# Optimization experiments

Measured on AMD Instinct MI355X. Metric: run time of the kernel, lower is better.

Reference implementation:

```python
import jax, jax.numpy as jnp
import numpy as np

N_NODES = 100000
N_EDGES = 1600000
IN_CH = 128
HID = 128
OUT_CH = 16
N_GRAPHS = 64


def setup_inputs() -> dict:
    key = jax.random.key(0)
    ks = jax.random.split(key, 8)
    x = jax.random.normal(ks[0], (N_NODES, IN_CH), dtype=jnp.float32)
    edge_index = jax.random.randint(ks[1], (2, N_EDGES), 0, N_NODES, dtype=jnp.int64)
    batch = jnp.sort(jax.random.randint(ks[2], (N_NODES,), 0, N_GRAPHS, dtype=jnp.int64))
    s1 = 1.0 / np.sqrt(IN_CH)
    s2 = 1.0 / np.sqrt(HID)
    W1 = jax.random.uniform(ks[3], (IN_CH, HID), jnp.float32, -s1, s1)
    b1 = jnp.zeros((HID,), jnp.float32)
    W2 = jax.random.uniform(ks[4], (HID, HID), jnp.float32, -s2, s2)
    b2 = jnp.zeros((HID,), jnp.float32)
    Wfc = jax.random.uniform(ks[5], (HID, OUT_CH), jnp.float32, -s2, s2)
    bfc = jax.random.uniform(ks[6], (OUT_CH,), jnp.float32, -s2, s2)
    return {"x": x, "W1": W1, "b1": b1, "W2": W2, "b2": b2,
            "Wfc": Wfc, "bfc": bfc, "edge_index": edge_index, "batch": batch}


def _gcn_conv(x, W, b, src, dst, deg_inv_sqrt, deg_inv):
    # GCNConv with self-loops: out = D^-1/2 (A+I) D^-1/2 (x W) + b
    h = x @ W                                   # [N, H]
    norm = deg_inv_sqrt[src] * deg_inv_sqrt[dst]  # [E]
    agg = jax.ops.segment_sum(h[src] * norm[:, None], dst, num_segments=N_NODES)
    # self-loop term: deg_inv_sqrt[i]^2 * h[i]
    return agg + h * deg_inv[:, None] + b


def reference(x, W1, b1, W2, b2, Wfc, bfc, edge_index, batch):
    src, dst = edge_index[0], edge_index[1]
    # degree including self-loop
    deg = jax.ops.segment_sum(jnp.ones((N_EDGES,), jnp.float32), dst, num_segments=N_NODES) + 1.0
    deg_inv_sqrt = jax.lax.rsqrt(deg)
    deg_inv = 1.0 / deg
    h = jax.nn.relu(_gcn_conv(x, W1, b1, src, dst, deg_inv_sqrt, deg_inv))
    h = jax.nn.relu(_gcn_conv(h, W2, b2, src, dst, deg_inv_sqrt, deg_inv))
    # global mean pool over graphs
    sums = jax.ops.segment_sum(h, batch, num_segments=N_GRAPHS)          # [G, H]
    counts = jax.ops.segment_sum(jnp.ones((N_NODES,), jnp.float32), batch, num_segments=N_GRAPHS)
    pooled = sums / jnp.maximum(counts, 1.0)[:, None]
    return pooled @ Wfc + bfc
```

## Files before the change

kernel.cpp:

```cpp
#include <hip/hip_runtime.h>
#include <math.h>

#define NN 100000
#define NE 1600000
#define CH 128
#define OUTC 16
#define NG 64

#define CBSH 8
#define NCB 391
#define CHK 4096
#define CAP 5120
#define NPW 8

typedef __attribute__((ext_vector_type(8))) short bf16x8;
typedef __attribute__((ext_vector_type(4))) float f32x4;

__device__ __forceinline__ unsigned short f2bf(float f) {
    union { float f; unsigned u; } v; v.f = f;
    unsigned r = v.u + 0x7FFF + ((v.u >> 16) & 1);
    return (unsigned short)(r >> 16);
}
__device__ __forceinline__ float bflo(unsigned u) {
    union { unsigned u; float f; } v; v.u = u << 16; return v.f;
}
__device__ __forceinline__ float bfhi(unsigned u) {
    union { unsigned u; float f; } v; v.u = u & 0xffff0000u; return v.f;
}

__device__ __forceinline__ float2 node_agg(const unsigned* __restrict__ base,
        const int* __restrict__ rowst, const int* __restrict__ degi,
        const int* __restrict__ csr, const float* __restrict__ dis,
        float bb0, float bb1, int n, int lane) {
    unsigned sv = base[(size_t)n * 64 + lane];
    float a0[8], a1[8];
    a0[0] = bflo(sv); a1[0] = bfhi(sv);
#pragma unroll
    for (int u = 1; u < 8; u++) { a0[u] = 0.f; a1[u] = 0.f; }
    int start = __builtin_amdgcn_readfirstlane(rowst[n]);
    int c = __builtin_amdgcn_readfirstlane(degi[n]);
    int j = 0;
    for (; j + 7 < c; j += 8) {
        int idx[8];
#pragma unroll
        for (int u = 0; u < 8; u++) idx[u] = csr[start + j + u];
        unsigned v[8];
#pragma unroll
        for (int u = 0; u < 8; u++) v[u] = base[(size_t)idx[u] * 64 + lane];
#pragma unroll
        for (int u = 0; u < 8; u++) { a0[u] += bflo(v[u]); a1[u] += bfhi(v[u]); }
    }
    for (; j < c; j++) {
        unsigned v0 = base[(size_t)csr[start + j] * 64 + lane];
        a0[j & 7] += bflo(v0); a1[j & 7] += bfhi(v0);
    }
#pragma unroll
    for (int off = 4; off >= 1; off >>= 1)
#pragma unroll
        for (int u = 0; u < off; u++) { a0[u] += a0[u + off]; a1[u] += a1[u + off]; }
    float d = dis[n];
    float ox = fmaxf(fmaf(d, a0[0], bb0), 0.f);
    float oy = fmaxf(fmaf(d, a1[0], bb1), 0.f);
    return make_float2(ox, oy);
}

__global__ void k_prep(const float* __restrict__ W1, const float* __restrict__ W2,
                       unsigned short* __restrict__ wt1, unsigned short* __restrict__ wt2,
                       const int* __restrict__ batch, int* __restrict__ gptr,
                       int* __restrict__ gfill, float* __restrict__ pooled) {
    int i = blockIdx.x * 256 + threadIdx.x;
    if (i < CH * CH) {
        int k = i >> 7, n = i & 127;
        wt1[n * CH + k] = f2bf(W1[i]);
    } else if (i < 2 * CH * CH) {
        int j = i - CH * CH;
        int k = j >> 7, n = j & 127;
        wt2[n * CH + k] = f2bf(W2[j]);
    }
    if (i < NCB) gfill[i] = 0;
    if (i < NG * CH) pooled[i] = 0.f;
    if (i < NN) {
        int b = batch[i];
        int prev = (i == 0) ? -1 : batch[i - 1];
        for (int g = prev + 1; g <= b; g++) gptr[g] = i;
        if (i == NN - 1) {
            for (int g = b + 1; g <= NG; g++) gptr[g] = NN;
        }
    }
}

__global__ __launch_bounds__(1024) void k_passA(const int* __restrict__ src, const int* __restrict__ dst,
                        int* __restrict__ gfill, unsigned* __restrict__ ebuf) {
    __shared__ unsigned lbuf[CHK];
    __shared__ unsigned short lb16[CHK];
    __shared__ int hcnt[NCB];
    __shared__ int hbase[512];
    __shared__ int goff[NCB];
    int t = threadIdx.x;
    if (t < NCB) hcnt[t] = 0;
    __syncthreads();
    int base = blockIdx.x * CHK;
    int cb[4], slot[4]; unsigned pk[4];
#pragma unroll
    for (int i = 0; i < 4; i++) {
        int e = base + i * 1024 + t;
        cb[i] = -1;
        if (e < NE) {
            int d = dst[e], s = src[e];
            cb[i] = d >> CBSH;
            pk[i] = ((unsigned)s << CBSH) | (unsigned)(d & (( 1 << CBSH) - 1));
            slot[i] = atomicAdd(&hcnt[cb[i]], 1);
        }
    }
    __syncthreads();
    if (t < 512) hbase[t] = (t < NCB) ? hcnt[t] : 0;
    __syncthreads();
    for (int off = 1; off < 512; off <<= 1) {
        int v = 0;
        if (t < 512 && t >= off) v = hbase[t - off];
        __syncthreads();
        if (t < 512) hbase[t] += v;
        __syncthreads();
    }
    if (t < NCB) {
        int c = hcnt[t];
        int g = c ? atomicAdd(&gfill[t], c) : 0;
        goff[t] = t * CAP + g - (hbase[t] - c);
    }
    __syncthreads();
#pragma unroll
    for (int i = 0; i < 4; i++) {
        if (cb[i] >= 0) {
            int pos = hbase[cb[i]] - hcnt[cb[i]] + slot[i];
            lbuf[pos] = pk[i];
            lb16[pos] = (unsigned short)cb[i];
        }
    }
    __syncthreads();
    int total = min(NE - base, CHK);
    for (int p = t; p < total; p += 1024) {
        unsigned v = lbuf[p];
        int b = lb16[p];
        ebuf[goff[b] + p] = v;
    }
}

__global__ __launch_bounds__(1024) void k_passB(const unsigned* __restrict__ ebuf, const int* __restrict__ gfill,
                        int* __restrict__ degi, int* __restrict__ rowst,
                        float* __restrict__ dis, int* __restrict__ csr) {
    __shared__ int cnt[256];
    __shared__ int nbase[256];
    __shared__ int fill[256];
    __shared__ int stage[CAP];
    int t = threadIdx.x;
    int cb = blockIdx.x;
    int nb0 = cb << CBSH;
    int ncnt = min(256, NN - nb0);
    int e0 = cb * CAP;
    int e1 = e0 + gfill[cb];
    if (t < 256) { cnt[t] = 0; fill[t] = 0; }
    __syncthreads();
    for (int e = e0 + t; e < e1; e += 1024)
        atomicAdd(&cnt[ebuf[e] & ((1 << CBSH) - 1)], 1);
    __syncthreads();
    if (t < 256) nbase[t] = cnt[t];
    __syncthreads();
    for (int off = 1; off < 256; off <<= 1) {
        int v = 0;
        if (t < 256 && t >= off) v = nbase[t - off];
        __syncthreads();
        if (t < 256) nbase[t] += v;
        __syncthreads();
    }
    for (int e = e0 + t; e < e1; e += 1024) {
        unsigned v = ebuf[e];
        int local = v & ((1 << CBSH) - 1);
        int s = atomicAdd(&fill[local], 1);
        stage[nbase[local] - cnt[local] + s] = (int)(v >> CBSH);
    }
    __syncthreads();
    int total = e1 - e0;
    for (int p = t; p < total; p += 1024) csr[e0 + p] = stage[p];
    if (t < ncnt) {
        int c = cnt[t];
        degi[nb0 + t] = c;
        rowst[nb0 + t] = e0 + nbase[t] - c;
        dis[nb0 + t] = rsqrtf((float)c + 1.0f);
    }
}

template<bool F32IN>
__launch_bounds__(256, 2)
__global__ void k_gemm(const void* __restrict__ Av,
                       const unsigned short* __restrict__ WT,
                       const float* __restrict__ dis,
                       unsigned short* __restrict__ out) {
    int tid = threadIdx.x;
    int wave = tid >> 6, lane = tid & 63;
    int quad = lane >> 4, l16 = lane & 15;

    int rbase = blockIdx.x * 128 + wave * 32;

    bf16x8 af[2][4];
#pragma unroll
    for (int s = 0; s < 2; s++) {
        int row = rbase + s * 16 + l16;
        if (row >= NN) row = NN - 1;
        if (F32IN) {
            const float* arow = (const float*)Av + (size_t)row * CH + quad * 8;
#pragma unroll
            for (int ks = 0; ks < 4; ks++) {
                float4 lo = *(const float4*)(arow + ks * 32);
                float4 hi = *(const float4*)(arow + ks * 32 + 4);
                union { bf16x8 v; unsigned short u[8]; } tmp;
                tmp.u[0] = f2bf(lo.x); tmp.u[1] = f2bf(lo.y);
                tmp.u[2] = f2bf(lo.z); tmp.u[3] = f2bf(lo.w);
                tmp.u[4] = f2bf(hi.x); tmp.u[5] = f2bf(hi.y);
                tmp.u[6] = f2bf(hi.z); tmp.u[7] = f2bf(hi.w);
                af[s][ks] = tmp.v;
            }
        } else {
            const unsigned short* arow = (const unsigned short*)Av + (size_t)row * CH + quad * 8;
#pragma unroll
            for (int ks = 0; ks < 4; ks++) af[s][ks] = *(const bf16x8*)(arow + ks * 32);
        }
    }

    f32x4 acc[2][8];
#pragma unroll
    for (int s = 0; s < 2; s++)
#pragma unroll
        for (int t = 0; t < 8; t++) acc[s][t] = (f32x4){0.f, 0.f, 0.f, 0.f};

#pragma unroll
    for (int t = 0; t < 8; t++) {
        const unsigned short* wcol = WT + (size_t)(t * 16 + l16) * CH + quad * 8;
        bf16x8 b0 = *(const bf16x8*)(wcol);
        bf16x8 b1 = *(const bf16x8*)(wcol + 32);
        bf16x8 b2 = *(const bf16x8*)(wcol + 64);
        bf16x8 b3 = *(const bf16x8*)(wcol + 96);
#pragma unroll
        for (int s = 0; s < 2; s++) {
            acc[s][t] = __builtin_amdgcn_mfma_f32_16x16x32_bf16(af[s][0], b0, acc[s][t], 0, 0, 0);
            acc[s][t] = __builtin_amdgcn_mfma_f32_16x16x32_bf16(af[s][1], b1, acc[s][t], 0, 0, 0);
            acc[s][t] = __builtin_amdgcn_mfma_f32_16x16x32_bf16(af[s][2], b2, acc[s][t], 0, 0, 0);
            acc[s][t] = __builtin_amdgcn_mfma_f32_16x16x32_bf16(af[s][3], b3, acc[s][t], 0, 0, 0);
        }
    }

#pragma unroll
    for (int s = 0; s < 2; s++) {
#pragma unroll
        for (int r = 0; r < 4; r++) {
            int orow = rbase + s * 16 + quad * 4 + r;
            if (orow < NN) {
                float d = dis[orow];
#pragma unroll
                for (int t = 0; t < 8; t++) {
                    out[(size_t)orow * CH + t * 16 + l16] = f2bf(acc[s][t][r] * d);
                }
            }
        }
    }
}

__global__ void k_agg(const unsigned short* __restrict__ ht, const int* __restrict__ rowst,
                      const int* __restrict__ degi, const int* __restrict__ csr,
                      const float* __restrict__ dis, const float* __restrict__ bias,
                      unsigned short* __restrict__ out) {
    int wave = threadIdx.x >> 6;
    int lane = threadIdx.x & 63;
    int n = blockIdx.x * 4 + wave;
    if (n >= NN) return;
    const unsigned* base = (const unsigned*)ht;
    float bb0 = bias[lane * 2], bb1 = bias[lane * 2 + 1];
    float2 o = node_agg(base, rowst, degi, csr, dis, bb0, bb1, n, lane);
    unsigned pk = ((unsigned)f2bf(o.y) << 16) | (unsigned)f2bf(o.x);
    ((unsigned*)out)[(size_t)n * 64 + lane] = pk;
}

__global__ void k_aggpool(const unsigned short* __restrict__ ht,
                          const int* __restrict__ rowst, const int* __restrict__ degi,
                          const int* __restrict__ csr, const float* __restrict__ dis,
                          const float* __restrict__ b2, const int* __restrict__ batch,
                          float* __restrict__ pooled) {
    int wave = threadIdx.x >> 6;
    int lane = threadIdx.x & 63;
    int n0 = (blockIdx.x * 4 + wave) * NPW;
    if (n0 >= NN) return;
    int n1 = n0 + NPW; if (n1 > NN) n1 = NN;
    const unsigned* base = (const unsigned*)ht;
    float bb0 = b2[lane * 2], bb1 = b2[lane * 2 + 1];
    float p0 = 0.f, p1 = 0.f;
    int gcur = __builtin_amdgcn_readfirstlane(batch[n0]);
    for (int n = n0; n < n1; n++) {
        int g = __builtin_amdgcn_readfirstlane(batch[n]);
        if (g != gcur) {
            atomicAdd(&pooled[gcur * CH + lane * 2],     p0);
            atomicAdd(&pooled[gcur * CH + lane * 2 + 1], p1);
            p0 = 0.f; p1 = 0.f; gcur = g;
        }
        float2 o = node_agg(base, rowst, degi, csr, dis, bb0, bb1, n, lane);
        p0 += o.x; p1 += o.y;
    }
    atomicAdd(&pooled[gcur * CH + lane * 2],     p0);
    atomicAdd(&pooled[gcur * CH + lane * 2 + 1], p1);
}

__global__ void k_final(const float* __restrict__ pooled, const int* __restrict__ gptr,
                        const float* __restrict__ Wfc, const float* __restrict__ bfc,
                        float* __restrict__ out) {
    int idx = blockIdx.x * 256 + threadIdx.x;
    if (idx >= NG * OUTC) return;
    int g = idx >> 4, o = idx & 15;
    float c = (float)(gptr[g + 1] - gptr[g]);
    float inv = 1.0f / fmaxf(c, 1.0f);
    float s = 0.f;
    for (int k = 0; k < CH; k++) s += pooled[g * CH + k] * Wfc[k * OUTC + o];
    out[idx] = fmaf(s, inv, bfc[o]);
}

extern "C" void kernel_launch(void* const* d_in, const int* in_sizes, int n_in,
                              void* d_out, int out_size, void* d_ws, size_t ws_size,
                              hipStream_t stream) {
    (void)in_sizes; (void)n_in; (void)out_size; (void)ws_size;
    const float* x   = (const float*)d_in[0];
    const float* W1  = (const float*)d_in[1];
    const float* b1  = (const float*)d_in[2];
    const float* W2  = (const float*)d_in[3];
    const float* b2  = (const float*)d_in[4];
    const float* Wfc = (const float*)d_in[5];
    const float* bfc = (const float*)d_in[6];
    const int* ei    = (const int*)d_in[7];
    const int* batch = (const int*)d_in[8];
    const int* esrc = ei;
    const int* edst = ei + NE;
    float* out = (float*)d_out;

    char* w = (char*)d_ws;
    unsigned short* bufA = (unsigned short*)w; w += (size_t)NN * CH * 2;
    unsigned short* bufB = (unsigned short*)w; w += (size_t)NN * CH * 2;
    unsigned short* wt1  = (unsigned short*)w; w += (size_t)CH * CH * 2;
    unsigned short* wt2  = (unsigned short*)w; w += (size_t)CH * CH * 2;
    unsigned* ebuf = (unsigned*)w; w += (size_t)NCB * CAP * 4;
    int* csr    = (int*)w;    w += (size_t)NCB * CAP * 4;
    int* degi   = (int*)w;    w += (size_t)NN * 4;
    int* rowst  = (int*)w;    w += (size_t)NN * 4;
    float* dis  = (float*)w;  w += (size_t)NN * 4;
    int* gfill  = (int*)w;    w += NCB * 4;
    int* gptr   = (int*)w;    w += (NG + 1) * 4;
    float* pooled = (float*)w; w += (size_t)NG * CH * 4;

    const int sortBlocks = (NE + CHK - 1) / CHK;
    const int rowBlocks  = (NN + 127) / 128;
    const int poolBlocks = (NN + 4 * NPW - 1) / (4 * NPW);

    k_prep<<<(NN + 255) / 256, 256, 0, stream>>>(W1, W2, wt1, wt2, batch, gptr, gfill, pooled);
    k_passA<<<sortBlocks, 1024, 0, stream>>>(esrc, edst, gfill, ebuf);
    k_passB<<<NCB, 1024, 0, stream>>>(ebuf, gfill, degi, rowst, dis, csr);

    k_gemm<true><<<rowBlocks, 256, 0, stream>>>(x, wt1, dis, bufA);
    k_agg<<<NN / 4, 256, 0, stream>>>(bufA, rowst, degi, csr, dis, b1, bufB);
    k_gemm<false><<<rowBlocks, 256, 0, stream>>>(bufB, wt2, dis, bufA);
    k_aggpool<<<poolBlocks, 256, 0, stream>>>(bufA, rowst, degi, csr, dis, b2, batch, pooled);

    k_final<<<(NG * OUTC + 255) / 256, 256, 0, stream>>>(pooled, gptr, Wfc, bfc, out);
}
```

Baseline: 334.3 us.

## Pad CSR rows to multiples of eight with a zero dummy node

Each CSR row is padded to a multiple of 8 entries whose index points at an extra zeroed row appended to bufA. The gather loop then always runs in full unrolled groups of 8 and the scalar tail loop is dropped. It also halves NPW, so the pooling aggregation launches more blocks with fewer nodes per wave. The cost is extra padded gathers of the dummy row, a larger CSR buffer and more shared memory in passB.

```diff
diff --git a/kernel.cpp b/kernel.cpp
--- a/kernel.cpp
+++ b/kernel.cpp
@@ -11,7 +11,8 @@
 #define NCB 391
 #define CHK 4096
 #define CAP 5120
-#define NPW 8
+#define CAPP 7168
+#define NPW 4
 
 typedef __attribute__((ext_vector_type(8))) short bf16x8;
 typedef __attribute__((ext_vector_type(4))) float f32x4;
@@ -39,8 +40,8 @@
     for (int u = 1; u < 8; u++) { a0[u] = 0.f; a1[u] = 0.f; }
     int start = __builtin_amdgcn_readfirstlane(rowst[n]);
     int c = __builtin_amdgcn_readfirstlane(degi[n]);
-    int j = 0;
-    for (; j + 7 < c; j += 8) {
+    int cp = (c + 7) & ~7;
+    for (int j = 0; j < cp; j += 8) {
         int idx[8];
 #pragma unroll
         for (int u = 0; u < 8; u++) idx[u] = csr[start + j + u];
@@ -49,10 +50,6 @@
         for (int u = 0; u < 8; u++) v[u] = base[(size_t)idx[u] * 64 + lane];
 #pragma unroll
         for (int u = 0; u < 8; u++) { a0[u] += bflo(v[u]); a1[u] += bfhi(v[u]); }
-    }
-    for (; j < c; j++) {
-        unsigned v0 = base[(size_t)csr[start + j] * 64 + lane];
-        a0[j & 7] += bflo(v0); a1[j & 7] += bfhi(v0);
     }
 #pragma unroll
     for (int off = 4; off >= 1; off >>= 1)
@@ -67,7 +64,8 @@
 __global__ void k_prep(const float* __restrict__ W1, const float* __restrict__ W2,
                        unsigned short* __restrict__ wt1, unsigned short* __restrict__ wt2,
                        const int* __restrict__ batch, int* __restrict__ gptr,
-                       int* __restrict__ gfill, float* __restrict__ pooled) {
+                       int* __restrict__ gfill, float* __restrict__ pooled,
+                       unsigned* __restrict__ bufAz) {
     int i = blockIdx.x * 256 + threadIdx.x;
     if (i < CH * CH) {
         int k = i >> 7, n = i & 127;
@@ -79,6 +77,7 @@
     }
     if (i < NCB) gfill[i] = 0;
     if (i < NG * CH) pooled[i] = 0.f;
+    if (i < 64) bufAz[(size_t)NN * 64 + i] = 0;
     if (i < NN) {
         int b = batch[i];
         int prev = (i == 0) ? -1 : batch[i - 1];
@@ -108,7 +107,7 @@
         if (e < NE) {
             int d = dst[e], s = src[e];
             cb[i] = d >> CBSH;
-            pk[i] = ((unsigned)s << CBSH) | (unsigned)(d & (( 1 << CBSH) - 1));
+            pk[i] = ((unsigned)s << CBSH) | (unsigned)(d & ((1 << CBSH) - 1));
             slot[i] = atomicAdd(&hcnt[cb[i]], 1);
         }
     }
@@ -149,9 +148,9 @@
                         int* __restrict__ degi, int* __restrict__ rowst,
                         float* __restrict__ dis, int* __restrict__ csr) {
     __shared__ int cnt[256];
-    __shared__ int nbase[256];
+    __shared__ int pb[256];
     __shared__ int fill[256];
-    __shared__ int stage[CAP];
+    __shared__ int stage[CAPP];
     int t = threadIdx.x;
     int cb = blockIdx.x;
     int nb0 = cb << CBSH;
@@ -163,30 +162,35 @@
     for (int e = e0 + t; e < e1; e += 1024)
         atomicAdd(&cnt[ebuf[e] & ((1 << CBSH) - 1)], 1);
     __syncthreads();
-    if (t < 256) nbase[t] = cnt[t];
+    if (t < 256) pb[t] = (cnt[t] + 7) & ~7;
     __syncthreads();
     for (int off = 1; off < 256; off <<= 1) {
         int v = 0;
-        if (t < 256 && t >= off) v = nbase[t - off];
+        if (t < 256 && t >= off) v = pb[t - off];
         __syncthreads();
-        if (t < 256) nbase[t] += v;
+        if (t < 256) pb[t] += v;
         __syncthreads();
     }
     for (int e = e0 + t; e < e1; e += 1024) {
         unsigned v = ebuf[e];
         int local = v & ((1 << CBSH) - 1);
         int s = atomicAdd(&fill[local], 1);
-        stage[nbase[local] - cnt[local] + s] = (int)(v >> CBSH);
-    }
-    __syncthreads();
-    int total = e1 - e0;
-    for (int p = t; p < total; p += 1024) csr[e0 + p] = stage[p];
+        int pc = (cnt[local] + 7) & ~7;
+        stage[pb[local] - pc + s] = (int)(v >> CBSH);
+    }
+    __syncthreads();
     if (t < ncnt) {
         int c = cnt[t];
+        int pc = (c + 7) & ~7;
+        int b = pb[t] - pc;
+        for (int k2 = c; k2 < pc; k2++) stage[b + k2] = NN;
         degi[nb0 + t] = c;
-        rowst[nb0 + t] = e0 + nbase[t] - c;
+        rowst[nb0 + t] = cb * CAPP + b;
         dis[nb0 + t] = rsqrtf((float)c + 1.0f);
     }
+    __syncthreads();
+    int ptotal = pb[255];
+    for (int p = t; p < ptotal; p += 1024) csr[(size_t)cb * CAPP + p] = stage[p];
 }
 
 template<bool F32IN>
@@ -338,12 +342,12 @@
     float* out = (float*)d_out;
 
     char* w = (char*)d_ws;
-    unsigned short* bufA = (unsigned short*)w; w += (size_t)NN * CH * 2;
+    unsigned short* bufA = (unsigned short*)w; w += (size_t)(NN + 1) * CH * 2;
     unsigned short* bufB = (unsigned short*)w; w += (size_t)NN * CH * 2;
     unsigned short* wt1  = (unsigned short*)w; w += (size_t)CH * CH * 2;
     unsigned short* wt2  = (unsigned short*)w; w += (size_t)CH * CH * 2;
     unsigned* ebuf = (unsigned*)w; w += (size_t)NCB * CAP * 4;
-    int* csr    = (int*)w;    w += (size_t)NCB * CAP * 4;
+    int* csr    = (int*)w;    w += (size_t)NCB * CAPP * 4;
     int* degi   = (int*)w;    w += (size_t)NN * 4;
     int* rowst  = (int*)w;    w += (size_t)NN * 4;
     float* dis  = (float*)w;  w += (size_t)NN * 4;
@@ -355,7 +359,8 @@
     const int rowBlocks  = (NN + 127) / 128;
     const int poolBlocks = (NN + 4 * NPW - 1) / (4 * NPW);
 
-    k_prep<<<(NN + 255) / 256, 256, 0, stream>>>(W1, W2, wt1, wt2, batch, gptr, gfill, pooled);
+    k_prep<<<(NN + 255) / 256, 256, 0, stream>>>(W1, W2, wt1, wt2, batch, gptr, gfill,
+                                                 pooled, (unsigned*)bufA);
     k_passA<<<sortBlocks, 1024, 0, stream>>>(esrc, edst, gfill, ebuf);
     k_passB<<<NCB, 1024, 0, stream>>>(ebuf, gfill, degi, rowst, dis, csr);
 
```

Measured after the change: 367.2 us. 9.8% more time.
